# Kernel optimization log

Hardware: AMD Instinct MI355X
Metric: run time of the kernel (lower is better)

Reference implementation:

```python
import jax, jax.numpy as jnp
from jax import lax
import numpy as np

T, B, I, H, L = 512, 256, 512, 256, 2  # seq, batch, input, hidden, layers per stack


def _param_shapes():
    # (stack, layer) -> input dim of that layer. Stack1 layer0 sees I, everything else sees H.
    shapes = []
    for s, in0 in enumerate([I, H]):
        for l in range(L):
            d_in = in0 if l == 0 else H
            shapes.append((f"s{s+1}l{l}", d_in))
    return shapes


def setup_inputs() -> dict:
    key = jax.random.key(0)
    d = {"x": jax.random.normal(jax.random.fold_in(key, 0), (T, B, I), jnp.float32)}
    k = 1.0 / np.sqrt(H)  # pytorch LSTM init scale
    i = 1
    for name, d_in in _param_shapes():
        d[name + "_wih"] = jax.random.uniform(jax.random.fold_in(key, i + 0), (4 * H, d_in), jnp.float32, -k, k)
        d[name + "_whh"] = jax.random.uniform(jax.random.fold_in(key, i + 1), (4 * H, H), jnp.float32, -k, k)
        d[name + "_bih"] = jax.random.uniform(jax.random.fold_in(key, i + 2), (4 * H,), jnp.float32, -k, k)
        d[name + "_bhh"] = jax.random.uniform(jax.random.fold_in(key, i + 3), (4 * H,), jnp.float32, -k, k)
        i += 4
    d["lr_w"] = jax.random.uniform(jax.random.fold_in(key, 100), (H, H), jnp.float32, -k, k)
    d["lr_b"] = jax.random.uniform(jax.random.fold_in(key, 101), (H,), jnp.float32, -k, k)
    return d


def _lstm_layer(x, wih, whh, bih, bhh):
    # x: (T, B, d_in) -> (T, B, H). PyTorch gate order: i, f, g, o.
    xg = jnp.einsum("tbi,gi->tbg", x, wih) + bih + bhh  # precompute input proj (T, B, 4H)
    h0 = jnp.zeros((x.shape[1], H), x.dtype)

    def step(carry, xt):
        h, c = carry
        g = xt + h @ whh.T
        gi, gf, gg, go = jnp.split(g, 4, axis=-1)
        c = jax.nn.sigmoid(gf) * c + jax.nn.sigmoid(gi) * jnp.tanh(gg)
        h = jax.nn.sigmoid(go) * jnp.tanh(c)
        return (h, c), h

    _, ys = lax.scan(step, (h0, h0), xg)
    return ys


def _forward(x, params, lr_w, lr_b):
    out = x
    for (wih, whh, bih, bhh) in params:
        out = _lstm_layer(out, wih, whh, bih, bhh)
    out = out @ lr_w.T + lr_b  # (T, B, H)
    return out[:, -1]  # faithful to original: index dim 1 (batch dim) -> (T, H)


def reference(x,
              s1l0_wih, s1l0_whh, s1l0_bih, s1l0_bhh,
              s1l1_wih, s1l1_whh, s1l1_bih, s1l1_bhh,
              s2l0_wih, s2l0_whh, s2l0_bih, s2l0_bhh,
              s2l1_wih, s2l1_whh, s2l1_bih, s2l1_bhh,
              lr_w, lr_b):
    params = [
        (s1l0_wih, s1l0_whh, s1l0_bih, s1l0_bhh),
        (s1l1_wih, s1l1_whh, s1l1_bih, s1l1_bhh),
        (s2l0_wih, s2l0_whh, s2l0_bih, s2l0_bhh),
        (s2l1_wih, s2l1_whh, s2l1_bih, s2l1_bhh),
    ]
    return _forward(x, params, lr_w, lr_b)
```

## Files before the change

kernel.cpp:

```cpp
#include <hip/hip_runtime.h>
#include <stdint.h>


typedef _Float16 half2v __attribute__((ext_vector_type(2)));

__device__ __forceinline__ float fdot2u(uint32_t w, uint32_t h, float acc) {
#if __has_builtin(__builtin_amdgcn_fdot2)
  return __builtin_amdgcn_fdot2(__builtin_bit_cast(half2v, w),
                                __builtin_bit_cast(half2v, h), acc, false);
#else
  half2v wv = __builtin_bit_cast(half2v, w);
  half2v hv = __builtin_bit_cast(half2v, h);
  acc += (float)wv[0] * (float)hv[0];
  acc += (float)wv[1] * (float)hv[1];
  return acc;
#endif
}

__device__ __forceinline__ float sigmoidf_(float x) {
  return 1.f / (1.f + __expf(-x));
}
__device__ __forceinline__ float tanhf_(float x) {
  return 1.f - 2.f / (__expf(2.f * x) + 1.f);
}

#define CNT_STRIDE 32

__device__ __forceinline__ int cnt_load(const int* p) {
  return __hip_atomic_load(p, __ATOMIC_RELAXED, __HIP_MEMORY_SCOPE_AGENT);
}
__device__ __forceinline__ void cnt_store(int* p, int v) {
  __hip_atomic_store(p, v, __ATOMIC_RELAXED, __HIP_MEMORY_SCOPE_AGENT);
}
__device__ __forceinline__ float ldg_f32(const float* p) {
  uint32_t u = __hip_atomic_load((const uint32_t*)p, __ATOMIC_RELAXED,
                                 __HIP_MEMORY_SCOPE_AGENT);
  return __builtin_bit_cast(float, u);
}
__device__ __forceinline__ void stg_f32(float* p, float v) {
  __hip_atomic_store((uint32_t*)p, __builtin_bit_cast(uint32_t, v),
                     __ATOMIC_RELAXED, __HIP_MEMORY_SCOPE_AGENT);
}
__device__ __forceinline__ uint64_t ldg_u64(const float* p) {
  return __hip_atomic_load((const uint64_t*)p, __ATOMIC_RELAXED,
                           __HIP_MEMORY_SCOPE_AGENT);
}

__device__ __forceinline__ void wait_ge(const int* p, int need, int& rdy) {
  while (rdy < need) {
    rdy = cnt_load(p);
    if (rdy < need) __builtin_amdgcn_s_sleep(2);
  }
  asm volatile("" ::: "memory");
}

__global__ void zero_cnt(int* c) {
  if (threadIdx.x < 16 * CNT_STRIDE) c[threadIdx.x] = 0;
}

__global__ __launch_bounds__(256) void pack_all(
    const float* __restrict__ w0, const float* __restrict__ w1,
    const float* __restrict__ w2, const float* __restrict__ w3,
    const float* __restrict__ w4, const float* __restrict__ w5,
    const float* __restrict__ w6, uint32_t* __restrict__ dst) {
  int b = blockIdx.x;
  int m = b >> 9;
  const float* src = (m == 0) ? w0 : (m == 1) ? w1 : (m == 2) ? w2
                   : (m == 3) ? w3 : (m == 4) ? w4 : (m == 5) ? w5 : w6;
  uint32_t* d = dst + (size_t)m * 131072;
  int idx = (b & 511) * 256 + threadIdx.x;
  int r = idx >> 7, k2 = idx & 127;
  float f0 = src[r * 256 + 2 * k2];
  float f1 = src[r * 256 + 2 * k2 + 1];
  union { _Float16 h; uint16_t u; } a, bb;
  a.h = (_Float16)f0;
  bb.h = (_Float16)f1;
  d[idx] = (uint32_t)a.u | ((uint32_t)bb.u << 16);
}

__global__ __launch_bounds__(256) void proj_gemm(const float* __restrict__ in, int istride, int K,
                                                 const float* __restrict__ W,
                                                 const float* __restrict__ bih,
                                                 const float* __restrict__ bhh,
                                                 float* __restrict__ xg) {
  __shared__ float xs[8][512];
  const int tid = threadIdx.x;
  const int r = blockIdx.x * 256 + tid;
  const int t0 = blockIdx.y * 8;
  for (int tt = 0; tt < 8; ++tt)
    for (int k = tid; k < K; k += 256)
      xs[tt][k] = in[(size_t)(t0 + tt) * istride + k];
  __syncthreads();
  float bias = bih[r] + bhh[r];
  float acc[8];
#pragma unroll
  for (int j = 0; j < 8; ++j) acc[j] = bias;
  const float* wr = W + (size_t)r * K;
  for (int k = 0; k < K; k += 4) {
    float4 w4 = *reinterpret_cast<const float4*>(wr + k);
#pragma unroll
    for (int j = 0; j < 8; ++j)
      acc[j] += xs[j][k] * w4.x + xs[j][k + 1] * w4.y + xs[j][k + 2] * w4.z +
                xs[j][k + 3] * w4.w;
  }
#pragma unroll
  for (int j = 0; j < 8; ++j) xg[(size_t)(t0 + j) * 1024 + r] = acc[j];
}


__device__ void scan_fn(int l, const uint32_t* __restrict__ wpk,
                        const float* __restrict__ xgsrc,
                        float* __restrict__ hseq, int* __restrict__ cnt) {
  __shared__ __align__(16) uint4 wlds[8 * 2 * 512];
  __shared__ __align__(16) uint16_t hbuf[2][256];
  const int tid = threadIdx.x;
  const int j = tid >> 1;
  const int odd = tid & 1;
  const int rA = j + (odd ? 512 : 0);
  const int rB = rA + 256;

  uint32_t wA[96], wB[96];
  {
    const uint4* gA = reinterpret_cast<const uint4*>(wpk + rA * 128);
    const uint4* gB = reinterpret_cast<const uint4*>(wpk + rB * 128);
#pragma unroll
    for (int q = 0; q < 24; ++q) {
      uint4 a = gA[q];
      wA[4 * q + 0] = a.x; wA[4 * q + 1] = a.y; wA[4 * q + 2] = a.z; wA[4 * q + 3] = a.w;
      uint4 b = gB[q];
      wB[4 * q + 0] = b.x; wB[4 * q + 1] = b.y; wB[4 * q + 2] = b.z; wB[4 * q + 3] = b.w;
    }
#pragma unroll
    for (int c = 0; c < 8; ++c) {
      wlds[(c * 2 + 0) * 512 + tid] = gA[24 + c];
      wlds[(c * 2 + 1) * 512 + tid] = gB[24 + c];
    }
  }
  if (tid < 256) hbuf[0][tid] = 0;
  __syncthreads();

  const int* mycnt = &cnt[(4 + (l - 1) * 2 + odd) * CNT_STRIDE];
  int rdy = 0;
  if (l) wait_ge(mycnt, 1, rdy);
  float c_ = 0.f;
  float xga = ldg_f32(xgsrc + rA), xgb = ldg_f32(xgsrc + rB);
  int pp = 0;
  for (int t = 0; t < 512; ++t) {
    const int tn = (t < 511) ? (t + 1) : 511;
    if (l) {
      int need = (t + 2 > 512) ? 512 : (t + 2);
      wait_ge(mycnt, need, rdy);
    }
    float nxa = ldg_f32(xgsrc + tn * 1024 + rA);
    float nxb = ldg_f32(xgsrc + tn * 1024 + rB);

    float accA0 = xga, accA1 = 0.f, accB0 = xgb, accB1 = 0.f;
    const uint4* hv4 = reinterpret_cast<const uint4*>(&hbuf[pp][0]);
#pragma unroll
    for (int ch = 0; ch < 24; ++ch) {
      uint4 h4 = hv4[ch];
      accA0 = fdot2u(wA[4 * ch + 0], h4.x, accA0);
      accA1 = fdot2u(wA[4 * ch + 1], h4.y, accA1);
      accA0 = fdot2u(wA[4 * ch + 2], h4.z, accA0);
      accA1 = fdot2u(wA[4 * ch + 3], h4.w, accA1);
      accB0 = fdot2u(wB[4 * ch + 0], h4.x, accB0);
      accB1 = fdot2u(wB[4 * ch + 1], h4.y, accB1);
      accB0 = fdot2u(wB[4 * ch + 2], h4.z, accB0);
      accB1 = fdot2u(wB[4 * ch + 3], h4.w, accB1);
    }
#pragma unroll
    for (int cc = 0; cc < 8; ++cc) {
      uint4 h4 = hv4[24 + cc];
      uint4 wa = wlds[(cc * 2 + 0) * 512 + tid];
      uint4 wb = wlds[(cc * 2 + 1) * 512 + tid];
      accA0 = fdot2u(wa.x, h4.x, accA0);
      accA1 = fdot2u(wa.y, h4.y, accA1);
      accA0 = fdot2u(wa.z, h4.z, accA0);
      accA1 = fdot2u(wa.w, h4.w, accA1);
      accB0 = fdot2u(wb.x, h4.x, accB0);
      accB1 = fdot2u(wb.y, h4.y, accB1);
      accB0 = fdot2u(wb.z, h4.z, accB0);
      accB1 = fdot2u(wb.w, h4.w, accB1);
    }
    float accA = accA0 + accA1;
    float accB = accB0 + accB1;

    float o0 = __shfl_xor(accA, 1);
    float o1 = __shfl_xor(accB, 1);
    float pi = odd ? o0 : accA;
    float pf = odd ? o1 : accB;
    float pg = odd ? accA : o0;
    float po = odd ? accB : o1;

    c_ = sigmoidf_(pf) * c_ + sigmoidf_(pi) * tanhf_(pg);
    float h = sigmoidf_(po) * tanhf_(c_);
    if (!odd) {
      stg_f32(hseq + t * 256 + j, h);
      union { _Float16 hf; uint16_t u; } cv;
      cv.hf = (_Float16)h;
      hbuf[pp ^ 1][j] = cv.u;
    }
    __syncthreads();
    if (tid == 0) cnt_store(&cnt[l * CNT_STRIDE], t + 1);
    pp ^= 1;
    xga = nxa;
    xgb = nxb;
  }
}

__device__ void proj_fn(int l, int half, const uint32_t* __restrict__ wpk,
                        const float* __restrict__ bih, const float* __restrict__ bhh,
                        const float* __restrict__ hsrc,
                        float* __restrict__ xgdst, int* __restrict__ cnt) {
  __shared__ __align__(16) uint32_t hpk[4][128];
  const int tid = threadIdx.x;
  const int row = half * 512 + tid;

  uint32_t wr_[128];
  {
    const uint4* g = reinterpret_cast<const uint4*>(wpk + (size_t)row * 128);
#pragma unroll
    for (int q = 0; q < 32; ++q) {
      uint4 v = g[q];
      wr_[4 * q + 0] = v.x; wr_[4 * q + 1] = v.y; wr_[4 * q + 2] = v.z; wr_[4 * q + 3] = v.w;
    }
  }
  const float bias = bih[row] + bhh[row];
  const int* prev = &cnt[(l - 1) * CNT_STRIDE];
  int* mine = &cnt[(4 + (l - 1) * 2 + half) * CNT_STRIDE];
  int rdy = 0;
  const int s4 = tid >> 7;
  const int c4 = tid & 127;

  for (int tt = 0; tt < 128; ++tt) {
    const int t0 = tt * 4;
    wait_ge(prev, t0 + 4, rdy);
    {
      uint64_t hv = ldg_u64(hsrc + (t0 + s4) * 256 + 2 * c4);
      float hx = __builtin_bit_cast(float, (uint32_t)hv);
      float hy = __builtin_bit_cast(float, (uint32_t)(hv >> 32));
      union { _Float16 h; uint16_t u; } a, b;
      a.h = (_Float16)hx;
      b.h = (_Float16)hy;
      hpk[s4][c4] = (uint32_t)a.u | ((uint32_t)b.u << 16);
    }
    __syncthreads();
#pragma unroll
    for (int s = 0; s < 4; ++s) {
      float a0 = bias, a1 = 0.f;
      const uint4* hv4 = reinterpret_cast<const uint4*>(hpk[s]);
#pragma unroll
      for (int q = 0; q < 32; ++q) {
        uint4 h4 = hv4[q];
        a0 = fdot2u(wr_[4 * q + 0], h4.x, a0);
        a1 = fdot2u(wr_[4 * q + 1], h4.y, a1);
        a0 = fdot2u(wr_[4 * q + 2], h4.z, a0);
        a1 = fdot2u(wr_[4 * q + 3], h4.w, a1);
      }
      stg_f32(xgdst + (t0 + s) * 1024 + row, a0 + a1);
    }
    __syncthreads();
    if (tid == 0) cnt_store(mine, t0 + 4);
  }
}

__device__ void final_fn(const float* __restrict__ lrw, const float* __restrict__ lrb,
                         const float* __restrict__ h3, float* __restrict__ out,
                         const int* __restrict__ cnt) {
  __shared__ __align__(16) float hs[256];
  const int tid = threadIdx.x;
  const int row = tid >> 1;
  const int kh = tid & 1;
  float w_[128];
  {
    const float4* g = reinterpret_cast<const float4*>(lrw + (size_t)row * 256 + kh * 128);
#pragma unroll
    for (int q = 0; q < 32; ++q) {
      float4 v = g[q];
      w_[4 * q + 0] = v.x; w_[4 * q + 1] = v.y; w_[4 * q + 2] = v.z; w_[4 * q + 3] = v.w;
    }
  }
  const float bias = lrb[row];
  const int* prev = &cnt[3 * CNT_STRIDE];
  int rdy = 0;
  for (int t = 0; t < 512; ++t) {
    wait_ge(prev, t + 1, rdy);
    if (tid < 128) {
      uint64_t hv = ldg_u64(h3 + t * 256 + 2 * tid);
      hs[2 * tid] = __builtin_bit_cast(float, (uint32_t)hv);
      hs[2 * tid + 1] = __builtin_bit_cast(float, (uint32_t)(hv >> 32));
    }
    __syncthreads();
    float a0 = 0.f, a1 = 0.f;
    const float* hp = hs + kh * 128;
#pragma unroll
    for (int k = 0; k < 128; k += 4) {
      a0 += w_[k] * hp[k] + w_[k + 2] * hp[k + 2];
      a1 += w_[k + 1] * hp[k + 1] + w_[k + 3] * hp[k + 3];
    }
    float s = a0 + a1;
    s += __shfl_xor(s, 1);
    if (!kh) out[t * 256 + row] = s + bias;
    __syncthreads();
  }
}

__global__ __launch_bounds__(512, 2) void pipeline(
    const uint32_t* __restrict__ wpkhh, const uint32_t* __restrict__ wpkih,
    const float* __restrict__ xg0, float* __restrict__ xgp,
    float* __restrict__ hseq,
    const float* __restrict__ bih1, const float* __restrict__ bhh1,
    const float* __restrict__ bih2, const float* __restrict__ bhh2,
    const float* __restrict__ bih3, const float* __restrict__ bhh3,
    const float* __restrict__ lrw, const float* __restrict__ lrb,
    float* __restrict__ out, int* __restrict__ cnt) {
  const int bx = blockIdx.x;
  if (bx == 0) {
    scan_fn(0, wpkhh, xg0, hseq, cnt);
  } else if (bx == 10) {
    final_fn(lrw, lrb, hseq + (size_t)3 * 131072, out, cnt);
  } else {
    const int g = bx - 1;
    const int l = g / 3 + 1;
    const int r = g % 3;
    const float* bih = (l == 1) ? bih1 : (l == 2) ? bih2 : bih3;
    const float* bhh = (l == 1) ? bhh1 : (l == 2) ? bhh2 : bhh3;
    if (r < 2)
      proj_fn(l, r, wpkih + (size_t)(l - 1) * 131072, bih, bhh,
              hseq + (size_t)(l - 1) * 131072, xgp + (size_t)(l - 1) * 524288, cnt);
    else
      scan_fn(l, wpkhh + (size_t)l * 131072, xgp + (size_t)(l - 1) * 524288,
              hseq + (size_t)l * 131072, cnt);
  }
}

extern "C" void kernel_launch(void* const* d_in, const int* in_sizes, int n_in,
                              void* d_out, int out_size, void* d_ws, size_t ws_size,
                              hipStream_t stream) {
  (void)in_sizes; (void)n_in; (void)out_size; (void)ws_size;
  const float* x = (const float*)d_in[0];
  const float* wih[4] = {(const float*)d_in[1], (const float*)d_in[5],
                         (const float*)d_in[9], (const float*)d_in[13]};
  const float* whh[4] = {(const float*)d_in[2], (const float*)d_in[6],
                         (const float*)d_in[10], (const float*)d_in[14]};
  const float* bih[4] = {(const float*)d_in[3], (const float*)d_in[7],
                         (const float*)d_in[11], (const float*)d_in[15]};
  const float* bhh[4] = {(const float*)d_in[4], (const float*)d_in[8],
                         (const float*)d_in[12], (const float*)d_in[16]};
  const float* lrw = (const float*)d_in[17];
  const float* lrb = (const float*)d_in[18];
  float* out = (float*)d_out;

  float* ws = (float*)d_ws;
  float* xg0 = ws;
  float* xgp = ws + 524288;
  float* hseq = xgp + 3 * 524288;
  uint32_t* wpkhh = (uint32_t*)(hseq + 4 * 131072);
  uint32_t* wpkih = wpkhh + 4 * 131072;
  int* cnt = (int*)(wpkih + 3 * 131072);

  zero_cnt<<<1, 512, 0, stream>>>(cnt);
  pack_all<<<3584, 256, 0, stream>>>(whh[0], whh[1], whh[2], whh[3],
                                     wih[1], wih[2], wih[3], wpkhh);

  proj_gemm<<<dim3(4, 64), 256, 0, stream>>>(x + 255 * 512, 256 * 512, 512,
                                             wih[0], bih[0], bhh[0], xg0);

  pipeline<<<11, 512, 0, stream>>>(wpkhh, wpkih, xg0, xgp, hseq,
                                   bih[1], bhh[1], bih[2], bhh[2], bih[3], bhh[3],
                                   lrw, lrb, out, cnt);
}
```

Before: 1.167 ms.

## Fuse fp16 weight packing into pipeline prologue and defer hseq stores

Removes the separate pack_all kernel launch and instead converts fp32 weights to packed fp16 while loading them into registers and LDS inside each pipeline block. The global store of h for step t is moved to the start of step t+1 so it leaves the critical path before the barrier. The published step counter is lowered by one to match, with a final store and count after the loop. This saves a launch and a round trip through the workspace, but doubles the bytes read in the prologue and adds a one-step lag to downstream consumers.

```diff
diff --git a/kernel.cpp b/kernel.cpp
--- a/kernel.cpp
+++ b/kernel.cpp
@@ -17,6 +17,13 @@
 #endif
 }
 
+__device__ __forceinline__ uint32_t pk2(float a, float b) {
+  union { _Float16 h; uint16_t u; } x, y;
+  x.h = (_Float16)a;
+  y.h = (_Float16)b;
+  return (uint32_t)x.u | ((uint32_t)y.u << 16);
+}
+
 __device__ __forceinline__ float sigmoidf_(float x) {
   return 1.f / (1.f + __expf(-x));
 }
@@ -56,26 +63,6 @@
 
 __global__ void zero_cnt(int* c) {
   if (threadIdx.x < 16 * CNT_STRIDE) c[threadIdx.x] = 0;
-}
-
-__global__ __launch_bounds__(256) void pack_all(
-    const float* __restrict__ w0, const float* __restrict__ w1,
-    const float* __restrict__ w2, const float* __restrict__ w3,
-    const float* __restrict__ w4, const float* __restrict__ w5,
-    const float* __restrict__ w6, uint32_t* __restrict__ dst) {
-  int b = blockIdx.x;
-  int m = b >> 9;
-  const float* src = (m == 0) ? w0 : (m == 1) ? w1 : (m == 2) ? w2
-                   : (m == 3) ? w3 : (m == 4) ? w4 : (m == 5) ? w5 : w6;
-  uint32_t* d = dst + (size_t)m * 131072;
-  int idx = (b & 511) * 256 + threadIdx.x;
-  int r = idx >> 7, k2 = idx & 127;
-  float f0 = src[r * 256 + 2 * k2];
-  float f1 = src[r * 256 + 2 * k2 + 1];
-  union { _Float16 h; uint16_t u; } a, bb;
-  a.h = (_Float16)f0;
-  bb.h = (_Float16)f1;
-  d[idx] = (uint32_t)a.u | ((uint32_t)bb.u << 16);
 }
 
 __global__ __launch_bounds__(256) void proj_gemm(const float* __restrict__ in, int istride, int K,
@@ -108,7 +95,7 @@
 }
 
 
-__device__ void scan_fn(int l, const uint32_t* __restrict__ wpk,
+__device__ void scan_fn(int l, const float* __restrict__ whh,
                         const float* __restrict__ xgsrc,
                         float* __restrict__ hseq, int* __restrict__ cnt) {
   __shared__ __align__(16) uint4 wlds[8 * 2 * 512];
@@ -121,19 +108,29 @@
 
   uint32_t wA[96], wB[96];
   {
-    const uint4* gA = reinterpret_cast<const uint4*>(wpk + rA * 128);
-    const uint4* gB = reinterpret_cast<const uint4*>(wpk + rB * 128);
+    const float4* gA = reinterpret_cast<const float4*>(whh + (size_t)rA * 256);
+    const float4* gB = reinterpret_cast<const float4*>(whh + (size_t)rB * 256);
 #pragma unroll
     for (int q = 0; q < 24; ++q) {
-      uint4 a = gA[q];
-      wA[4 * q + 0] = a.x; wA[4 * q + 1] = a.y; wA[4 * q + 2] = a.z; wA[4 * q + 3] = a.w;
-      uint4 b = gB[q];
-      wB[4 * q + 0] = b.x; wB[4 * q + 1] = b.y; wB[4 * q + 2] = b.z; wB[4 * q + 3] = b.w;
+      float4 a0 = gA[2 * q], a1 = gA[2 * q + 1];
+      wA[4 * q + 0] = pk2(a0.x, a0.y); wA[4 * q + 1] = pk2(a0.z, a0.w);
+      wA[4 * q + 2] = pk2(a1.x, a1.y); wA[4 * q + 3] = pk2(a1.z, a1.w);
+      float4 b0 = gB[2 * q], b1 = gB[2 * q + 1];
+      wB[4 * q + 0] = pk2(b0.x, b0.y); wB[4 * q + 1] = pk2(b0.z, b0.w);
+      wB[4 * q + 2] = pk2(b1.x, b1.y); wB[4 * q + 3] = pk2(b1.z, b1.w);
     }
 #pragma unroll
     for (int c = 0; c < 8; ++c) {
-      wlds[(c * 2 + 0) * 512 + tid] = gA[24 + c];
-      wlds[(c * 2 + 1) * 512 + tid] = gB[24 + c];
+      float4 t0 = gA[48 + 2 * c], t1 = gA[49 + 2 * c];
+      uint4 v;
+      v.x = pk2(t0.x, t0.y); v.y = pk2(t0.z, t0.w);
+      v.z = pk2(t1.x, t1.y); v.w = pk2(t1.z, t1.w);
+      wlds[(c * 2 + 0) * 512 + tid] = v;
+      float4 u0 = gB[48 + 2 * c], u1 = gB[49 + 2 * c];
+      uint4 w;
+      w.x = pk2(u0.x, u0.y); w.y = pk2(u0.z, u0.w);
+      w.z = pk2(u1.x, u1.y); w.w = pk2(u1.z, u1.w);
+      wlds[(c * 2 + 1) * 512 + tid] = w;
     }
   }
   if (tid < 256) hbuf[0][tid] = 0;
@@ -144,6 +141,7 @@
   if (l) wait_ge(mycnt, 1, rdy);
   float c_ = 0.f;
   float xga = ldg_f32(xgsrc + rA), xgb = ldg_f32(xgsrc + rB);
+  float hprev = 0.f;
   int pp = 0;
   for (int t = 0; t < 512; ++t) {
     const int tn = (t < 511) ? (t + 1) : 511;
@@ -151,6 +149,7 @@
       int need = (t + 2 > 512) ? 512 : (t + 2);
       wait_ge(mycnt, need, rdy);
     }
+    if (!odd && t > 0) stg_f32(hseq + (t - 1) * 256 + j, hprev);
     float nxa = ldg_f32(xgsrc + tn * 1024 + rA);
     float nxb = ldg_f32(xgsrc + tn * 1024 + rB);
 
@@ -195,20 +194,23 @@
     c_ = sigmoidf_(pf) * c_ + sigmoidf_(pi) * tanhf_(pg);
     float h = sigmoidf_(po) * tanhf_(c_);
     if (!odd) {
-      stg_f32(hseq + t * 256 + j, h);
       union { _Float16 hf; uint16_t u; } cv;
       cv.hf = (_Float16)h;
       hbuf[pp ^ 1][j] = cv.u;
     }
-    __syncthreads();
-    if (tid == 0) cnt_store(&cnt[l * CNT_STRIDE], t + 1);
+    hprev = h;
+    __syncthreads();
+    if (tid == 0) cnt_store(&cnt[l * CNT_STRIDE], t);
     pp ^= 1;
     xga = nxa;
     xgb = nxb;
   }
-}
-
-__device__ void proj_fn(int l, int half, const uint32_t* __restrict__ wpk,
+  if (!odd) stg_f32(hseq + 511 * 256 + j, hprev);
+  __syncthreads();
+  if (tid == 0) cnt_store(&cnt[l * CNT_STRIDE], 512);
+}
+
+__device__ void proj_fn(int l, int half, const float* __restrict__ wih,
                         const float* __restrict__ bih, const float* __restrict__ bhh,
                         const float* __restrict__ hsrc,
                         float* __restrict__ xgdst, int* __restrict__ cnt) {
@@ -218,11 +220,12 @@
 
   uint32_t wr_[128];
   {
-    const uint4* g = reinterpret_cast<const uint4*>(wpk + (size_t)row * 128);
+    const float4* g = reinterpret_cast<const float4*>(wih + (size_t)row * 256);
 #pragma unroll
     for (int q = 0; q < 32; ++q) {
-      uint4 v = g[q];
-      wr_[4 * q + 0] = v.x; wr_[4 * q + 1] = v.y; wr_[4 * q + 2] = v.z; wr_[4 * q + 3] = v.w;
+      float4 f0 = g[2 * q], f1 = g[2 * q + 1];
+      wr_[4 * q + 0] = pk2(f0.x, f0.y); wr_[4 * q + 1] = pk2(f0.z, f0.w);
+      wr_[4 * q + 2] = pk2(f1.x, f1.y); wr_[4 * q + 3] = pk2(f1.z, f1.w);
     }
   }
   const float bias = bih[row] + bhh[row];
@@ -239,10 +242,7 @@
       uint64_t hv = ldg_u64(hsrc + (t0 + s4) * 256 + 2 * c4);
       float hx = __builtin_bit_cast(float, (uint32_t)hv);
       float hy = __builtin_bit_cast(float, (uint32_t)(hv >> 32));
-      union { _Float16 h; uint16_t u; } a, b;
-      a.h = (_Float16)hx;
-      b.h = (_Float16)hy;
-      hpk[s4][c4] = (uint32_t)a.u | ((uint32_t)b.u << 16);
+      hpk[s4][c4] = pk2(hx, hy);
     }
     __syncthreads();
 #pragma unroll
@@ -287,8 +287,10 @@
     wait_ge(prev, t + 1, rdy);
     if (tid < 128) {
       uint64_t hv = ldg_u64(h3 + t * 256 + 2 * tid);
-      hs[2 * tid] = __builtin_bit_cast(float, (uint32_t)hv);
-      hs[2 * tid + 1] = __builtin_bit_cast(float, (uint32_t)(hv >> 32));
+      uint2 u;
+      u.x = (uint32_t)hv;
+      u.y = (uint32_t)(hv >> 32);
+      *reinterpret_cast<uint2*>(&hs[2 * tid]) = u;
     }
     __syncthreads();
     float a0 = 0.f, a1 = 0.f;
@@ -306,7 +308,10 @@
 }
 
 __global__ __launch_bounds__(512, 2) void pipeline(
-    const uint32_t* __restrict__ wpkhh, const uint32_t* __restrict__ wpkih,
+    const float* __restrict__ whh0, const float* __restrict__ whh1,
+    const float* __restrict__ whh2, const float* __restrict__ whh3,
+    const float* __restrict__ wih1, const float* __restrict__ wih2,
+    const float* __restrict__ wih3,
     const float* __restrict__ xg0, float* __restrict__ xgp,
     float* __restrict__ hseq,
     const float* __restrict__ bih1, const float* __restrict__ bhh1,
@@ -316,20 +321,22 @@
     float* __restrict__ out, int* __restrict__ cnt) {
   const int bx = blockIdx.x;
   if (bx == 0) {
-    scan_fn(0, wpkhh, xg0, hseq, cnt);
+    scan_fn(0, whh0, xg0, hseq, cnt);
   } else if (bx == 10) {
     final_fn(lrw, lrb, hseq + (size_t)3 * 131072, out, cnt);
   } else {
     const int g = bx - 1;
     const int l = g / 3 + 1;
     const int r = g % 3;
+    const float* whh = (l == 1) ? whh1 : (l == 2) ? whh2 : whh3;
+    const float* wih = (l == 1) ? wih1 : (l == 2) ? wih2 : wih3;
     const float* bih = (l == 1) ? bih1 : (l == 2) ? bih2 : bih3;
     const float* bhh = (l == 1) ? bhh1 : (l == 2) ? bhh2 : bhh3;
     if (r < 2)
-      proj_fn(l, r, wpkih + (size_t)(l - 1) * 131072, bih, bhh,
+      proj_fn(l, r, wih, bih, bhh,
               hseq + (size_t)(l - 1) * 131072, xgp + (size_t)(l - 1) * 524288, cnt);
     else
-      scan_fn(l, wpkhh + (size_t)l * 131072, xgp + (size_t)(l - 1) * 524288,
+      scan_fn(l, whh, xgp + (size_t)(l - 1) * 524288,
               hseq + (size_t)l * 131072, cnt);
   }
 }
@@ -355,18 +362,16 @@
   float* xg0 = ws;
   float* xgp = ws + 524288;
   float* hseq = xgp + 3 * 524288;
-  uint32_t* wpkhh = (uint32_t*)(hseq + 4 * 131072);
-  uint32_t* wpkih = wpkhh + 4 * 131072;
-  int* cnt = (int*)(wpkih + 3 * 131072);
+  int* cnt = (int*)(hseq + 4 * 131072);
 
   zero_cnt<<<1, 512, 0, stream>>>(cnt);
-  pack_all<<<3584, 256, 0, stream>>>(whh[0], whh[1], whh[2], whh[3],
-                                     wih[1], wih[2], wih[3], wpkhh);
 
   proj_gemm<<<dim3(4, 64), 256, 0, stream>>>(x + 255 * 512, 256 * 512, 512,
                                              wih[0], bih[0], bhh[0], xg0);
 
-  pipeline<<<11, 512, 0, stream>>>(wpkhh, wpkih, xg0, xgp, hseq,
+  pipeline<<<11, 512, 0, stream>>>(whh[0], whh[1], whh[2], whh[3],
+                                   wih[1], wih[2], wih[3],
+                                   xg0, xgp, hseq,
                                    bih[1], bhh[1], bih[2], bhh[2], bih[3], bhh[3],
                                    lrw, lrb, out, cnt);
 }
```

After: 1.199 ms. 1.03x slower.
